# Optimization experiments

Hardware: AMD Instinct MI355X
Metric: run time of the kernel (lower is better)

The kernel has to match this reference:

```python
import jax, jax.numpy as jnp
import numpy as np

CUTOFF = 5.0
BOX = 20.0
EPS = 1e-5


def _neighbor_list_np(cutoff, coords, cell):
    # coords: [N,3] float32, cell: [3,3]. Returns (pair_first, pair_second, pair_image)
    inv_cell = np.linalg.inv(cell)
    proj = coords @ inv_cell
    frac = np.fmod(proj, 1.0)                      # matches torch.fmod (sign-preserving)
    woff = np.floor(proj).astype(np.int64)          # torch.div(..., rounding_mode='floor')
    wrapped = (frac @ cell).astype(coords.dtype)
    inv_lengths = np.linalg.norm(inv_cell, axis=0)
    nb = (np.floor(cutoff * inv_lengths + EPS) + 1).astype(np.int64)
    ranges = [np.arange(-int(n), int(n) + 1) for n in nb]
    # image grid ordered (i1 outer, i2, i3 inner) to match the nested torch loops
    images = np.stack(np.meshgrid(*ranges, indexing='ij'), axis=-1).reshape(-1, 3)
    off_cart = images.astype(coords.dtype) @ cell   # [K,3]
    drij = wrapped[:, None, :] - wrapped[None, :, :]           # [N,N,3]
    diff = drij[None, :, :, :] + off_cart[:, None, None, :]    # [K,N,N,3]
    dist = np.linalg.norm(diff, axis=-1)                       # [K,N,N]
    mask = dist < cutoff
    zero_k = int(np.where((images == 0).all(axis=1))[0][0])
    np.fill_diagonal(mask[zero_k], False)                      # drop self pairs in home image
    k, i, j = np.nonzero(mask)  # row-major (k,i,j) == per-image blocks of (i,j), same order as torch
    woff_ij = woff[i] - woff[j]
    pair_image = images[k] - woff_ij
    return i, j, pair_image


def setup_inputs() -> dict:
    key = jax.random.key(0)
    n_mol, n_at = 16, 512
    coordinates = jax.random.uniform(key, (n_mol, n_at, 3), dtype=jnp.float32) * BOX
    nonblank = jnp.ones((n_mol, n_at), dtype=bool)
    real_atoms = jnp.arange(n_mol * n_at, dtype=jnp.int32)
    inv_real_atoms = jnp.arange(n_mol * n_at, dtype=jnp.int32)
    cell = jnp.tile((BOX * jnp.eye(3, dtype=jnp.float32))[None], (n_mol, 1, 1))
    mol_index = jnp.arange(n_mol * n_at, dtype=jnp.int32) // n_at
    return dict(coordinates=coordinates, nonblank=nonblank, real_atoms=real_atoms,
                inv_real_atoms=inv_real_atoms, cell=cell, mol_index=mol_index,
                n_molecules=n_mol, n_atoms_max=n_at)


def reference(coordinates, nonblank, real_atoms, inv_real_atoms, cell, mol_index,
              n_molecules, n_atoms_max):
    # --- neighbor-list construction (torch.no_grad section): host numpy, vectorized over images ---
    coords_np = np.asarray(coordinates)
    cell_np = np.asarray(cell)
    nb_np = np.asarray(nonblank)
    pfs, pss, ofs = [], [], []
    for m in range(n_molecules):
        r = coords_np[m][nb_np[m]]
        pf, ps, of = _neighbor_list_np(CUTOFF, r, cell_np[m])
        if len(pf) == 0:
            continue
        pfs.append(pf + m * n_atoms_max)
        pss.append(ps + m * n_atoms_max)
        ofs.append(of)
    pf = np.concatenate(pfs)
    ps = np.concatenate(pss)
    of = np.concatenate(ofs)
    n_images = max(1, int(np.abs(of).max()))

    pair_first = inv_real_atoms[jnp.asarray(pf)]
    pair_second = inv_real_atoms[jnp.asarray(ps)]
    offsets = jnp.asarray(of.astype(np.int32))
    n_off = 2 * n_images + 1
    o1, o2, o3 = (offsets + n_images).T
    offset_index = o3 + n_off * (o2 + n_off * o1)
    pair_mol = mol_index[pair_first]
    pair_cell = cell[pair_mol]                                   # [P,3,3]
    pair_offsets = jnp.einsum('pk,pkl->pl', offsets.astype(cell.dtype), pair_cell)

    # --- differentiable distance evaluation ---
    coordflat = coordinates.reshape(n_molecules * n_atoms_max, 3)[real_atoms]
    paircoord = coordflat[pair_first] - coordflat[pair_second] + pair_offsets
    distflat2 = jnp.linalg.norm(paircoord, axis=1)
    return distflat2, pair_first, pair_second, paircoord, offsets, offset_index
```

## Files before the change

### kernel.cpp

```cpp
#include <hip/hip_runtime.h>

#define NMOL 16
#define NAT  512
#define NK   27

#define SSMAX 24.999998092651367f

__device__ __forceinline__ float wrap1(float v) {
    return __fmul_rn(__fmul_rn(v, 0.05f), 20.0f);
}

__device__ __forceinline__ bool probe(float dx, float dy, float dz,
                                      int& ox, int& oy, int& oz,
                                      float& cx, float& cy, float& cz) {
    ox = (dx > 15.0f) ? -1 : ((dx < -15.0f) ? 1 : 0);
    oy = (dy > 15.0f) ? -1 : ((dy < -15.0f) ? 1 : 0);
    oz = (dz > 15.0f) ? -1 : ((dz < -15.0f) ? 1 : 0);
    cx = 20.0f * (float)ox;
    cy = 20.0f * (float)oy;
    cz = 20.0f * (float)oz;
    float ax = __fadd_rn(dx, cx);
    float ay = __fadd_rn(dy, cy);
    float az = __fadd_rn(dz, cz);
    float ss = __fadd_rn(__fadd_rn(__fmul_rn(ax, ax), __fmul_rn(ay, ay)),
                         __fmul_rn(az, az));
    return ss < SSMAX;
}

__global__ __launch_bounds__(256, 8) void pass_count(const float* __restrict__ coords,
                                                     int* __restrict__ cnt) {
    __shared__ float w4[NAT * 4];
    __shared__ int   cur[4][NK];
    const int blk = blockIdx.x;
    const int m   = blk >> 7;
    const int ig  = blk & 127;
    const int t   = threadIdx.x;
    const int w   = t >> 6;
    const int lane = t & 63;
    const int i   = ig * 4 + w;

    const float* cm = coords + (size_t)m * NAT * 3;
    for (int q = t; q < NAT * 3; q += 256) {
        int a = q / 3, c = q - a * 3;
        w4[a * 4 + c] = wrap1(cm[q]);
    }
    if (t < 4 * NK) cur[t / NK][t % NK] = 0;
    __syncthreads();

    const float wx = w4[i * 4 + 0];
    const float wy = w4[i * 4 + 1];
    const float wz = w4[i * 4 + 2];
    const float4* w4p = reinterpret_cast<const float4*>(w4);

    #pragma unroll
    for (int it = 0; it < NAT / 64; ++it) {
        const int j = it * 64 + lane;
        float4 wj = w4p[j];
        float dx = __fsub_rn(wx, wj.x);
        float dy = __fsub_rn(wy, wj.y);
        float dz = __fsub_rn(wz, wj.z);
        int ox, oy, oz; float cx, cy, cz;
        bool hit = probe(dx, dy, dz, ox, oy, oz, cx, cy, cz) && (j != i);
        if (hit) {
            int k = (ox + 1) * 9 + (oy + 1) * 3 + (oz + 1);
            atomicAdd(&cur[w][k], 1);
        }
    }
    __syncthreads();

    if (t < 4 * NK) {
        int ww = t / NK, k = t % NK;
        cnt[(m * NK + k) * NAT + (ig * 4 + ww)] = cur[ww][k];
    }
}

__global__ __launch_bounds__(512) void scan_chunk(int* __restrict__ cnt,
                                                  int* __restrict__ sums) {
    __shared__ int buf[512];
    const int c = blockIdx.x;
    const int t = threadIdx.x;
    const int idx = c * 512 + t;
    buf[t] = cnt[idx];
    __syncthreads();
    for (int d = 1; d < 512; d <<= 1) {
        int v = (t >= d) ? buf[t - d] : 0;
        __syncthreads();
        buf[t] += v;
        __syncthreads();
    }
    cnt[idx] = (t == 0) ? 0 : buf[t - 1];
    if (t == 511) sums[c] = buf[511];
}

__global__ __launch_bounds__(256, 8) void pass_emit(const float* __restrict__ coords,
                                                    const int* __restrict__ cnt,
                                                    const int* __restrict__ sums,
                                                    float* __restrict__ out, int P) {
    __shared__ float w4[NAT * 4];
    __shared__ float r4[NAT * 4];
    __shared__ int   sbuf[512];
    __shared__ int   cur[4][NK];
    const int blk = blockIdx.x;
    const int m   = blk >> 7;
    const int ig  = blk & 127;
    const int t   = threadIdx.x;
    const int w   = t >> 6;
    const int lane = t & 63;
    const int i   = ig * 4 + w;

    const float* cm = coords + (size_t)m * NAT * 3;
    for (int q = t; q < NAT * 3; q += 256) {
        int a = q / 3, c = q - a * 3;
        float v = cm[q];
        r4[a * 4 + c] = v;
        w4[a * 4 + c] = wrap1(v);
    }
    {
        int v0 = (t < NMOL * NK) ? sums[t] : 0;
        int t2 = t + 256;
        int v1 = (t2 < NMOL * NK) ? sums[t2] : 0;
        sbuf[t] = v0;
        sbuf[t2] = v1;
    }
    __syncthreads();
    for (int d = 1; d < 512; d <<= 1) {
        int a0 = (t >= d) ? sbuf[t - d] : 0;
        int t2 = t + 256;
        int a1 = sbuf[t2 - d];
        __syncthreads();
        sbuf[t]  += a0;
        sbuf[t2] += a1;
        __syncthreads();
    }
    if (t < 4 * NK) {
        int ww = t / NK, k = t % NK;
        int c  = m * NK + k;
        int gbase = (c == 0) ? 0 : sbuf[c - 1];
        cur[ww][k] = cnt[c * NAT + (ig * 4 + ww)] + gbase;
    }
    __syncthreads();

    const float wx = w4[i * 4 + 0];
    const float wy = w4[i * 4 + 1];
    const float wz = w4[i * 4 + 2];
    const float rx = r4[i * 4 + 0];
    const float ry = r4[i * 4 + 1];
    const float rz = r4[i * 4 + 2];
    const float4* w4p = reinterpret_cast<const float4*>(w4);
    const float4* r4p = reinterpret_cast<const float4*>(r4);
    const int pf = m * NAT + i;
    const unsigned long long ltmask =
        (lane == 0) ? 0ull : (~0ull >> (64 - lane));

    for (int it = 0; it < NAT / 64; ++it) {
        const int j = it * 64 + lane;
        float4 wj = w4p[j];
        float dx = __fsub_rn(wx, wj.x);
        float dy = __fsub_rn(wy, wj.y);
        float dz = __fsub_rn(wz, wj.z);
        int ox, oy, oz; float cx, cy, cz;
        bool hit = probe(dx, dy, dz, ox, oy, oz, cx, cy, cz) && (j != i);
        int kk = hit ? ((ox + 1) * 9 + (oy + 1) * 3 + (oz + 1)) : 0;

        unsigned long long grp = __ballot(hit);
        #pragma unroll
        for (int b = 0; b < 5; ++b) {
            unsigned long long bm = __ballot((kk >> b) & 1);
            grp &= ((kk >> b) & 1) ? bm : ~bm;
        }
        int leader = hit ? (__ffsll((unsigned long long)grp) - 1) : 0;
        int cntg   = __popcll(grp);
        int rank   = __popcll(grp & ltmask);

        int base = 0;
        if (hit && lane == leader)
            base = atomicAdd(&cur[w][kk], cntg);
        base = __shfl(base, leader, 64);

        if (hit) {
            int p = base + rank;
            if (p < P) {
                float4 rj = r4p[j];
                float px = __fadd_rn(__fsub_rn(rx, rj.x), cx);
                float py = __fadd_rn(__fsub_rn(ry, rj.y), cy);
                float pz = __fadd_rn(__fsub_rn(rz, rj.z), cz);
                float ss = __fadd_rn(__fadd_rn(__fmul_rn(px, px), __fmul_rn(py, py)),
                                     __fmul_rn(pz, pz));
                out[p]                 = __fsqrt_rn(ss);
                out[P + p]             = (float)pf;
                out[2 * P + p]         = (float)(m * NAT + j);
                out[3 * P + 3 * p + 0] = px;
                out[3 * P + 3 * p + 1] = py;
                out[3 * P + 3 * p + 2] = pz;
                out[6 * P + 3 * p + 0] = (float)ox;
                out[6 * P + 3 * p + 1] = (float)oy;
                out[6 * P + 3 * p + 2] = (float)oz;
                out[9 * P + p]         = (float)kk;
            }
        }
    }
}

extern "C" void kernel_launch(void* const* d_in, const int* in_sizes, int n_in,
                              void* d_out, int out_size, void* d_ws, size_t ws_size,
                              hipStream_t stream) {
    const float* coords = (const float*)d_in[0];
    int* cnt  = (int*)d_ws;
    int* sums = cnt + NMOL * NK * NAT;
    float* out = (float*)d_out;
    const int P = out_size / 10;

    hipLaunchKernelGGL(pass_count, dim3(NMOL * NAT / 4), dim3(256), 0, stream, coords, cnt);
    hipLaunchKernelGGL(scan_chunk, dim3(NMOL * NK), dim3(512), 0, stream, cnt, sums);
    hipLaunchKernelGGL(pass_emit, dim3(NMOL * NAT / 4), dim3(256), 0, stream,
                       coords, cnt, sums, out, P);
}
```

Measured before the change: 96.12 us.

## Cache per-thread hit codes from count pass to skip recomputing distances in emit

The count pass now packs each thread's 8 hit flags and image indices into a 64-bit code and writes it to workspace. The emit pass reads that code instead of re-wrapping coordinates and re-running the distance probe, which drops the wrapped-coordinate shared array and the probe arithmetic. In exchange it adds a 2 MB global write and read of the codes, and it relies on the workspace being large enough to hold them.

```diff
diff --git a/kernel.cpp b/kernel.cpp
--- a/kernel.cpp
+++ b/kernel.cpp
@@ -3,6 +3,7 @@
 #define NMOL 16
 #define NAT  512
 #define NK   27
+#define NCHUNK (NMOL * NK)
 
 #define SSMAX 24.999998092651367f
 
@@ -11,24 +12,21 @@
 }
 
 __device__ __forceinline__ bool probe(float dx, float dy, float dz,
-                                      int& ox, int& oy, int& oz,
-                                      float& cx, float& cy, float& cz) {
+                                      int& ox, int& oy, int& oz) {
     ox = (dx > 15.0f) ? -1 : ((dx < -15.0f) ? 1 : 0);
     oy = (dy > 15.0f) ? -1 : ((dy < -15.0f) ? 1 : 0);
     oz = (dz > 15.0f) ? -1 : ((dz < -15.0f) ? 1 : 0);
-    cx = 20.0f * (float)ox;
-    cy = 20.0f * (float)oy;
-    cz = 20.0f * (float)oz;
-    float ax = __fadd_rn(dx, cx);
-    float ay = __fadd_rn(dy, cy);
-    float az = __fadd_rn(dz, cz);
+    float ax = __fadd_rn(dx, 20.0f * (float)ox);
+    float ay = __fadd_rn(dy, 20.0f * (float)oy);
+    float az = __fadd_rn(dz, 20.0f * (float)oz);
     float ss = __fadd_rn(__fadd_rn(__fmul_rn(ax, ax), __fmul_rn(ay, ay)),
                          __fmul_rn(az, az));
     return ss < SSMAX;
 }
 
 __global__ __launch_bounds__(256, 8) void pass_count(const float* __restrict__ coords,
-                                                     int* __restrict__ cnt) {
+                                                     int* __restrict__ cnt,
+                                                     unsigned long long* __restrict__ codes) {
     __shared__ float w4[NAT * 4];
     __shared__ int   cur[4][NK];
     const int blk = blockIdx.x;
@@ -52,6 +50,7 @@
     const float wz = w4[i * 4 + 2];
     const float4* w4p = reinterpret_cast<const float4*>(w4);
 
+    unsigned long long code = 0ull;
     #pragma unroll
     for (int it = 0; it < NAT / 64; ++it) {
         const int j = it * 64 + lane;
@@ -59,13 +58,15 @@
         float dx = __fsub_rn(wx, wj.x);
         float dy = __fsub_rn(wy, wj.y);
         float dz = __fsub_rn(wz, wj.z);
-        int ox, oy, oz; float cx, cy, cz;
-        bool hit = probe(dx, dy, dz, ox, oy, oz, cx, cy, cz) && (j != i);
+        int ox, oy, oz;
+        bool hit = probe(dx, dy, dz, ox, oy, oz) && (j != i);
         if (hit) {
-            int k = (ox + 1) * 9 + (oy + 1) * 3 + (oz + 1);
-            atomicAdd(&cur[w][k], 1);
+            int kk = (ox + 1) * 9 + (oy + 1) * 3 + (oz + 1);
+            code |= ((unsigned long long)(0x20 | kk)) << (6 * it);
+            atomicAdd(&cur[w][kk], 1);
         }
     }
+    codes[(size_t)blk * 256 + t] = code;
     __syncthreads();
 
     if (t < 4 * NK) {
@@ -95,8 +96,8 @@
 __global__ __launch_bounds__(256, 8) void pass_emit(const float* __restrict__ coords,
                                                     const int* __restrict__ cnt,
                                                     const int* __restrict__ sums,
+                                                    const unsigned long long* __restrict__ codes,
                                                     float* __restrict__ out, int P) {
-    __shared__ float w4[NAT * 4];
     __shared__ float r4[NAT * 4];
     __shared__ int   sbuf[512];
     __shared__ int   cur[4][NK];
@@ -108,28 +109,27 @@
     const int lane = t & 63;
     const int i   = ig * 4 + w;
 
+    const unsigned long long code = codes[(size_t)blk * 256 + t];
+
     const float* cm = coords + (size_t)m * NAT * 3;
     for (int q = t; q < NAT * 3; q += 256) {
         int a = q / 3, c = q - a * 3;
-        float v = cm[q];
-        r4[a * 4 + c] = v;
-        w4[a * 4 + c] = wrap1(v);
+        r4[a * 4 + c] = cm[q];
     }
     {
-        int v0 = (t < NMOL * NK) ? sums[t] : 0;
+        int v0 = (t < NCHUNK) ? sums[t] : 0;
         int t2 = t + 256;
-        int v1 = (t2 < NMOL * NK) ? sums[t2] : 0;
-        sbuf[t] = v0;
+        int v1 = (t2 < NCHUNK) ? sums[t2] : 0;
+        sbuf[t]  = v0;
         sbuf[t2] = v1;
     }
     __syncthreads();
     for (int d = 1; d < 512; d <<= 1) {
         int a0 = (t >= d) ? sbuf[t - d] : 0;
-        int t2 = t + 256;
-        int a1 = sbuf[t2 - d];
-        __syncthreads();
-        sbuf[t]  += a0;
-        sbuf[t2] += a1;
+        int a1 = sbuf[t + 256 - d];
+        __syncthreads();
+        sbuf[t]       += a0;
+        sbuf[t + 256] += a1;
         __syncthreads();
     }
     if (t < 4 * NK) {
@@ -140,27 +140,18 @@
     }
     __syncthreads();
 
-    const float wx = w4[i * 4 + 0];
-    const float wy = w4[i * 4 + 1];
-    const float wz = w4[i * 4 + 2];
     const float rx = r4[i * 4 + 0];
     const float ry = r4[i * 4 + 1];
     const float rz = r4[i * 4 + 2];
-    const float4* w4p = reinterpret_cast<const float4*>(w4);
     const float4* r4p = reinterpret_cast<const float4*>(r4);
     const int pf = m * NAT + i;
     const unsigned long long ltmask =
         (lane == 0) ? 0ull : (~0ull >> (64 - lane));
 
     for (int it = 0; it < NAT / 64; ++it) {
-        const int j = it * 64 + lane;
-        float4 wj = w4p[j];
-        float dx = __fsub_rn(wx, wj.x);
-        float dy = __fsub_rn(wy, wj.y);
-        float dz = __fsub_rn(wz, wj.z);
-        int ox, oy, oz; float cx, cy, cz;
-        bool hit = probe(dx, dy, dz, ox, oy, oz, cx, cy, cz) && (j != i);
-        int kk = hit ? ((ox + 1) * 9 + (oy + 1) * 3 + (oz + 1)) : 0;
+        const int v    = (int)((code >> (6 * it)) & 0x3F);
+        const bool hit = (v & 0x20) != 0;
+        const int kk   = v & 0x1F;
 
         unsigned long long grp = __ballot(hit);
         #pragma unroll
@@ -180,10 +171,14 @@
         if (hit) {
             int p = base + rank;
             if (p < P) {
+                const int j  = it * 64 + lane;
+                const int ox = kk / 9 - 1;
+                const int oy = (kk / 3) % 3 - 1;
+                const int oz = kk % 3 - 1;
                 float4 rj = r4p[j];
-                float px = __fadd_rn(__fsub_rn(rx, rj.x), cx);
-                float py = __fadd_rn(__fsub_rn(ry, rj.y), cy);
-                float pz = __fadd_rn(__fsub_rn(rz, rj.z), cz);
+                float px = __fadd_rn(__fsub_rn(rx, rj.x), 20.0f * (float)ox);
+                float py = __fadd_rn(__fsub_rn(ry, rj.y), 20.0f * (float)oy);
+                float pz = __fadd_rn(__fsub_rn(rz, rj.z), 20.0f * (float)oz);
                 float ss = __fadd_rn(__fadd_rn(__fmul_rn(px, px), __fmul_rn(py, py)),
                                      __fmul_rn(pz, pz));
                 out[p]                 = __fsqrt_rn(ss);
@@ -207,11 +202,14 @@
     const float* coords = (const float*)d_in[0];
     int* cnt  = (int*)d_ws;
     int* sums = cnt + NMOL * NK * NAT;
+    unsigned long long* codes =
+        (unsigned long long*)(cnt + NMOL * NK * NAT + 512);
     float* out = (float*)d_out;
     const int P = out_size / 10;
 
-    hipLaunchKernelGGL(pass_count, dim3(NMOL * NAT / 4), dim3(256), 0, stream, coords, cnt);
-    hipLaunchKernelGGL(scan_chunk, dim3(NMOL * NK), dim3(512), 0, stream, cnt, sums);
+    hipLaunchKernelGGL(pass_count, dim3(NMOL * NAT / 4), dim3(256), 0, stream,
+                       coords, cnt, codes);
+    hipLaunchKernelGGL(scan_chunk, dim3(NCHUNK), dim3(512), 0, stream, cnt, sums);
     hipLaunchKernelGGL(pass_emit, dim3(NMOL * NAT / 4), dim3(256), 0, stream,
-                       coords, cnt, sums, out, P);
-}
+                       coords, cnt, sums, codes, out, P);
+}
```

After: 97.37 us. No clear change (+1.3%).
